# Kernel tuning notes

Measured on AMD Instinct MI355X. Metric: run time of the kernel, lower is better.

## Reference

```python
import jax, jax.numpy as jnp
import numpy as np

NUM_HEADS = 16


def setup_inputs() -> dict:
    key = jax.random.key(0)
    ks = jax.random.split(key, 5)
    S, B, N, C = 4, 2, 2048, 1024
    return {
        "x_all": jax.random.normal(ks[0], (S, B, N, C), dtype=jnp.float32),
        "w_qkv": jax.random.normal(ks[1], (C, 3 * C), dtype=jnp.float32) * (C ** -0.5),
        "b_qkv": jax.random.normal(ks[2], (3 * C,), dtype=jnp.float32) * 0.02,
        "w_proj": jax.random.normal(ks[3], (C, C), dtype=jnp.float32) * (C ** -0.5),
        "b_proj": jax.random.normal(ks[4], (C,), dtype=jnp.float32) * 0.02,
    }


def reference(x_all, w_qkv, b_qkv, w_proj, b_proj):
    # x_all: [S, B, N, C] -- S = cp_dim ring shards, each rank holds [B, N, C]
    S, B, N, C = x_all.shape
    H = NUM_HEADS
    D = C // H
    scale = 1.0 / np.sqrt(D).astype(np.float32)

    # same qkv projection on every rank
    qkv = (jnp.einsum("sbnc,ce->sbne", x_all, w_qkv) + b_qkv)
    qkv = qkv.reshape(S, B, N, 3, H, D)
    # rank 0's queries: [B, H, N, D]
    q = jnp.transpose(qkv[0, :, :, 0], (0, 2, 1, 3))
    # all shards' keys/values: [S, B, H, N, D]
    k = jnp.transpose(qkv[:, :, :, 1], (0, 1, 3, 2, 4))
    v = jnp.transpose(qkv[:, :, :, 2], (0, 1, 3, 2, 4))

    # ring loop: online softmax merge across KV shards (numerically stable
    # form of the source's exp(lse)-weighted average)
    attn_out, lse = None, None
    for s in range(S):
        scores = jnp.einsum("bhnd,bhmd->bhnm", q, k[s]) * scale  # [B,H,N,N]
        new_lse = jax.nn.logsumexp(scores, axis=-1)               # [B,H,N]
        probs = jnp.exp(scores - new_lse[..., None])
        new_out = jnp.einsum("bhnm,bhmd->bhnd", probs, v[s])      # [B,H,N,D]
        if attn_out is None:
            attn_out, lse = new_out, new_lse
        else:
            m = jnp.logaddexp(lse, new_lse)
            attn_out = (attn_out * jnp.exp(lse - m)[..., None]
                        + new_out * jnp.exp(new_lse - m)[..., None])
            lse = m

    # [B,H,N,D] -> [B,N,C]
    out = jnp.transpose(attn_out, (0, 2, 1, 3)).reshape(B, N, C)
    return out @ w_proj + b_proj
```

## Files before the change

### kernel.cpp

```cpp
#include <hip/hip_runtime.h>
#include <hip/hip_bf16.h>


typedef __bf16 bf16x8 __attribute__((ext_vector_type(8)));
typedef float v4f __attribute__((ext_vector_type(4)));

#if __has_builtin(__builtin_amdgcn_exp2f)
#define EXP2F(x) __builtin_amdgcn_exp2f(x)
#else
#define EXP2F(x) exp2f(x)
#endif

__device__ __forceinline__ float bf2f(unsigned short h) {
  union { unsigned int u; float f; } a; a.u = ((unsigned int)h) << 16; return a.f;
}
__device__ __forceinline__ unsigned short f2bf(float f) {
  union { float f; unsigned int u; } a; a.f = f;
  unsigned int u = a.u;
  unsigned int r = (u + 0x7fffu + ((u >> 16) & 1u)) >> 16;
  return (unsigned short)r;
}
__device__ __forceinline__ unsigned int pack2t(float a, float b) {
  union { float f; unsigned int u; } ua, ub; ua.f = a; ub.f = b;
  return (ua.u >> 16) | (ub.u & 0xffff0000u);
}
__device__ __forceinline__ bf16x8 ldfrag16(const unsigned short* p) {
  union { uint4 u; bf16x8 v; } x; x.u = *(const uint4*)p; return x.v;
}
__device__ __forceinline__ bf16x8 ones8() {
  union { unsigned short s[8]; bf16x8 v; } x;
#pragma unroll
  for (int i = 0; i < 8; i++) x.s[i] = 0x3F80;
  return x.v;
}
__device__ __forceinline__ void gld_lds16(const unsigned short* g, unsigned short* l) {
  __builtin_amdgcn_global_load_lds((__attribute__((address_space(1))) void*)g,
                                   (__attribute__((address_space(3))) void*)l, 16, 0, 0);
}

__global__ void detect_dtype(const unsigned short* __restrict__ x, int* flag) {
  __shared__ int cnt;
  if (threadIdx.x == 0) cnt = 0;
  __syncthreads();
  int sane = 0;
#pragma unroll
  for (int j = 0; j < 4; j++) {
    unsigned short v = x[2 * (threadIdx.x + 64 * j)];
    int e = (v >> 7) & 0xFF;
    if (e >= 90 && e <= 140) sane++;
  }
  atomicAdd(&cnt, sane);
  __syncthreads();
  if (threadIdx.x == 0) *flag = (cnt > 160) ? 0 : 1;
}

__global__ void conv_to_bf16(const void* __restrict__ in, unsigned short* __restrict__ out,
                             int n4, const int* __restrict__ flag) {
  int i = blockIdx.x * blockDim.x + threadIdx.x;
  if (i >= n4) return;
  if (*flag) {
    float4 v = ((const float4*)in)[i];
    ushort4 o;
    o.x = f2bf(v.x); o.y = f2bf(v.y); o.z = f2bf(v.z); o.w = f2bf(v.w);
    ((ushort4*)out)[i] = o;
  } else {
    ((ushort4*)out)[i] = ((const ushort4*)in)[i];
  }
}

__global__ void conv_bias(const void* __restrict__ bq_in, const void* __restrict__ bp_in,
                          unsigned short* __restrict__ bq, unsigned short* __restrict__ bp,
                          const int* __restrict__ flag) {
  int i = blockIdx.x * 256 + threadIdx.x;
  const void* in = (i < 768) ? bq_in : bp_in;
  unsigned short* out = (i < 768) ? bq : bp;
  int j = (i < 768) ? i : i - 768;
  if (*flag) {
    float4 v = ((const float4*)in)[j];
    ushort4 o;
    o.x = f2bf(v.x); o.y = f2bf(v.y); o.z = f2bf(v.z); o.w = f2bf(v.w);
    ((ushort4*)out)[j] = o;
  } else {
    ((ushort4*)out)[j] = ((const ushort4*)in)[j];
  }
}

__global__ void trans_both(const void* __restrict__ wqkv, const void* __restrict__ wproj,
                           unsigned short* __restrict__ wt1, unsigned short* __restrict__ wt2,
                           const int* __restrict__ flag) {
  __shared__ unsigned short t[32][33];
  int tx = threadIdx.x, ty = threadIdx.y;
  int bx = blockIdx.x;
  const void* in; unsigned short* out; int C, c0;
  if (bx < 96) { in = wqkv; out = wt1; C = 3072; c0 = bx * 32; }
  else         { in = wproj; out = wt2; C = 1024; c0 = (bx - 96) * 32; }
  const int R = 1024;
  int r0 = blockIdx.y * 32;
  int fp = *flag;
#pragma unroll
  for (int j = 0; j < 32; j += 8) {
    unsigned short v;
    if (fp) v = f2bf(((const float*)in)[(r0 + ty + j) * C + c0 + tx]);
    else    v = ((const unsigned short*)in)[(r0 + ty + j) * C + c0 + tx];
    t[ty + j][tx] = v;
  }
  __syncthreads();
#pragma unroll
  for (int j = 0; j < 32; j += 8) out[(c0 + ty + j) * R + r0 + tx] = t[tx][ty + j];
}

template <int MODE>
__launch_bounds__(256, 3)
__global__ void gemm_bt(const unsigned short* __restrict__ A,
                        const unsigned short* __restrict__ Bt,
                        const unsigned short* __restrict__ bias,
                        void* __restrict__ Cout,
                        int K, int ldc, const int* __restrict__ flag,
                        const unsigned short* Bt2, const unsigned short* bias2,
                        void* Cout2) {
  __shared__ unsigned short As[128 * 32];
  __shared__ unsigned short Bs[128 * 32];
  int tid = threadIdx.x;
  int w = tid >> 6, lane = tid & 63, col = lane & 15, quad = lane >> 4;
  int wm = w >> 1, wn = w & 1;
  int n0 = blockIdx.x * 128;
  int m0 = blockIdx.y * 128;
  const unsigned short* Bt_ = Bt;
  const unsigned short* bias_ = bias;
  void* Cout_ = Cout;
  bool isq = false;
  if constexpr (MODE == 3) {
    if (blockIdx.y >= 128) {
      m0 = (blockIdx.y - 128) * 128;
      Bt_ = Bt2; bias_ = bias2; Cout_ = Cout2;
      isq = true;
    }
  }
  int fp = 0;
  if constexpr (MODE == 2) fp = *flag;

  v4f acc[4][4];
#pragma unroll
  for (int i = 0; i < 4; i++)
#pragma unroll
    for (int j = 0; j < 4; j++) acc[i][j] = v4f{0.f, 0.f, 0.f, 0.f};

  int ra0 = tid >> 2, cc = tid & 3;
  const unsigned short* ga0 = &A[(m0 + ra0) * K + cc * 8];
  const unsigned short* ga1 = ga0 + 64 * K;
  const unsigned short* gb0 = &Bt_[(n0 + ra0) * K + cc * 8];
  const unsigned short* gb1 = gb0 + 64 * K;
  unsigned short* lA0 = &As[(w * 16) * 32];
  unsigned short* lA1 = &As[(64 + w * 16) * 32];
  unsigned short* lB0 = &Bs[(w * 16) * 32];
  unsigned short* lB1 = &Bs[(64 + w * 16) * 32];

  int niter = K >> 5;
  for (int it = 0; it < niter; it++) {
    __syncthreads();
    gld_lds16(ga0, lA0); gld_lds16(ga1, lA1);
    gld_lds16(gb0, lB0); gld_lds16(gb1, lB1);
    ga0 += 32; ga1 += 32; gb0 += 32; gb1 += 32;
    __syncthreads();
    bf16x8 af[4], bfr[4];
#pragma unroll
    for (int mi = 0; mi < 4; mi++) af[mi] = ldfrag16(&As[(wm * 64 + mi * 16 + col) * 32 + quad * 8]);
#pragma unroll
    for (int ni = 0; ni < 4; ni++) bfr[ni] = ldfrag16(&Bs[(wn * 64 + ni * 16 + col) * 32 + quad * 8]);
#pragma unroll
    for (int mi = 0; mi < 4; mi++)
#pragma unroll
      for (int ni = 0; ni < 4; ni++)
        acc[mi][ni] = __builtin_amdgcn_mfma_f32_16x16x32_bf16(af[mi], bfr[ni], acc[mi][ni], 0, 0, 0);
  }

  float bv[4];
#pragma unroll
  for (int ni = 0; ni < 4; ni++) bv[ni] = bf2f(bias_[n0 + wn * 64 + ni * 16 + col]);

  if constexpr (MODE == 1) {
    int rgb0 = m0 + wm * 64;
    int s = rgb0 >> 12, b = (rgb0 >> 11) & 1, n = rgb0 & 2047;
    int kvg0 = s * 2048 + n;
#pragma unroll
    for (int ni = 0; ni < 4; ni++) {
      int cg = n0 + wn * 64 + ni * 16 + col;
      int h = cg >> 6, d = cg & 63;
      unsigned short* rowp = &((unsigned short*)Cout_)[((b * 16 + h) * 64 + d) * 8192 + kvg0];
      float bvn = bv[ni];
#pragma unroll
      for (int r = 0; r < 4; r++) {
        ushort2 e, o2;
        e.x = f2bf(acc[0][ni][r] + bvn);
        e.y = f2bf(acc[2][ni][r] + bvn);
        o2.x = f2bf(acc[1][ni][r] + bvn);
        o2.y = f2bf(acc[3][ni][r] + bvn);
        *(ushort2*)&rowp[2 * (quad * 4 + r)] = e;
        *(ushort2*)&rowp[32 + 2 * (quad * 4 + r)] = o2;
      }
    }
  } else {
#pragma unroll
    for (int mi = 0; mi < 4; mi++)
#pragma unroll
      for (int ni = 0; ni < 4; ni++) {
        float vals[4];
#pragma unroll
        for (int r = 0; r < 4; r++) vals[r] = acc[mi][ni][r] + bv[ni];
        if constexpr (MODE == 3) {
          if (isq) {
#pragma unroll
            for (int r = 0; r < 4; r++) vals[r] *= 0.1803368801111601f;
          }
        }
        int rgb = m0 + wm * 64 + mi * 16 + quad * 4;
        int cg  = n0 + wn * 64 + ni * 16 + col;
        if constexpr (MODE == 0 || MODE == 3) {
          unsigned short* C = (unsigned short*)Cout_;
#pragma unroll
          for (int r = 0; r < 4; r++) C[(rgb + r) * ldc + cg] = f2bf(vals[r]);
        } else {
          if (fp) {
            float* C = (float*)Cout_;
#pragma unroll
            for (int r = 0; r < 4; r++) C[(rgb + r) * ldc + cg] = vals[r];
          } else {
            unsigned short* C = (unsigned short*)Cout_;
#pragma unroll
            for (int r = 0; r < 4; r++) C[(rgb + r) * ldc + cg] = f2bf(vals[r]);
          }
        }
      }
  }
}

__launch_bounds__(512, 4)
__global__ void attn_kernel(const unsigned short* __restrict__ qbuf,
                            const unsigned short* __restrict__ kbuf,
                            const unsigned short* __restrict__ vt,
                            float* __restrict__ po,
                            float* __restrict__ lbuf) {
  __shared__ unsigned short Ks[2][64 * 64];
  __shared__ unsigned short Vs[2][64 * 64];
  int tid = threadIdx.x;
  int w = tid >> 6, lane = tid & 63, col = lane & 15, quad = lane >> 4;
  int id = blockIdx.x;
  int xcd = id & 7, slot = id >> 3;
  int qt = slot & 7, gsub = slot >> 3;
  int g = gsub * 8 + xcd;
  int bh = g >> 1, half = g & 1;
  int b = bh >> 4, h = bh & 15;
  int q0 = qt * 256;

  bf16x8 aQ[2][2];
#pragma unroll
  for (int mj = 0; mj < 2; mj++)
#pragma unroll
    for (int kk = 0; kk < 2; kk++)
      aQ[mj][kk] = ldfrag16(&qbuf[(b * 2048 + q0 + w * 32 + mj * 16 + col) * 1024 +
                                  h * 64 + kk * 32 + quad * 8]);

  int r0 = tid >> 3, c0 = tid & 7;
  const unsigned short* kp = &kbuf[((half * 2) * 4096 + b * 2048 + r0) * 1024 + h * 64 + c0 * 8];
  const unsigned short* vp = &vt[(bh * 64 + r0) * 8192 + half * 4096 + c0 * 8];
  int sdst = r0 * 64 + 8 * (c0 ^ (r0 & 7));
  {
    uint4 k0 = *(const uint4*)kp, v0 = *(const uint4*)vp;
    *(uint4*)&Ks[0][sdst] = k0;
    *(uint4*)&Vs[0][sdst] = v0;
  }

  const bf16x8 vone = ones8();
  v4f o[2][4];
  v4f acc_l[2] = {v4f{0.f, 0.f, 0.f, 0.f}, v4f{0.f, 0.f, 0.f, 0.f}};
#pragma unroll
  for (int mj = 0; mj < 2; mj++)
#pragma unroll
    for (int di = 0; di < 4; di++) o[mj][di] = v4f{0.f, 0.f, 0.f, 0.f};

  __syncthreads();

  for (int kvt = 0; kvt < 64; kvt++) {
    int p = kvt & 1;
    uint4 pk, pv;
    if (kvt < 63) {
      int kstep = (((kvt + 1) & 31) == 0) ? (2048 + 64) * 1024 : 64 * 1024;
      kp += kstep; vp += 64;
      pk = *(const uint4*)kp; pv = *(const uint4*)vp;
    }

    v4f sc[4][2];
#pragma unroll
    for (int ni = 0; ni < 4; ni++)
#pragma unroll
      for (int mj = 0; mj < 2; mj++) sc[ni][mj] = v4f{0.f, 0.f, 0.f, 0.f};
#pragma unroll
    for (int kk = 0; kk < 2; kk++) {
      bf16x8 aK[4];
#pragma unroll
      for (int ni = 0; ni < 4; ni++) {
        int row = ni * 16 + col;
        aK[ni] = ldfrag16(&Ks[p][row * 64 + 8 * ((kk * 4 + quad) ^ (col & 7))]);
      }
#pragma unroll
      for (int ni = 0; ni < 4; ni++)
#pragma unroll
        for (int mj = 0; mj < 2; mj++)
          sc[ni][mj] = __builtin_amdgcn_mfma_f32_16x16x32_bf16(aK[ni], aQ[mj][kk], sc[ni][mj], 0, 0, 0);
    }

#pragma unroll
    for (int ni = 0; ni < 4; ni++)
#pragma unroll
      for (int mj = 0; mj < 2; mj++)
#pragma unroll
        for (int r = 0; r < 4; r++) sc[ni][mj][r] = EXP2F(sc[ni][mj][r]);

    bf16x8 aP[2][2];
#pragma unroll
    for (int mj = 0; mj < 2; mj++)
#pragma unroll
      for (int kk = 0; kk < 2; kk++) {
        union { unsigned int d[4]; bf16x8 v; } u;
#pragma unroll
        for (int t = 0; t < 4; t++)
          u.d[t] = pack2t(sc[kk][mj][t], sc[kk + 2][mj][t]);
        aP[mj][kk] = u.v;
      }

    if (kvt < 63) {
      *(uint4*)&Ks[p ^ 1][sdst] = pk;
      *(uint4*)&Vs[p ^ 1][sdst] = pv;
    }

#pragma unroll
    for (int kk = 0; kk < 2; kk++) {
#pragma unroll
      for (int mj = 0; mj < 2; mj++)
        acc_l[mj] = __builtin_amdgcn_mfma_f32_16x16x32_bf16(aP[mj][kk], vone, acc_l[mj], 0, 0, 0);
      bf16x8 bV[4];
#pragma unroll
      for (int di = 0; di < 4; di++) {
        int row = di * 16 + col;
        bV[di] = ldfrag16(&Vs[p][row * 64 + 8 * ((kk * 4 + quad) ^ (col & 7))]);
      }
#pragma unroll
      for (int mj = 0; mj < 2; mj++)
#pragma unroll
        for (int di = 0; di < 4; di++)
          o[mj][di] = __builtin_amdgcn_mfma_f32_16x16x32_bf16(aP[mj][kk], bV[di], o[mj][di], 0, 0, 0);
    }

    __syncthreads();
  }

  float* pb = po + half * 4194304;
#pragma unroll
  for (int mj = 0; mj < 2; mj++)
#pragma unroll
    for (int r = 0; r < 4; r++) {
      int n = q0 + w * 32 + mj * 16 + quad * 4 + r;
      if (col == 0) lbuf[half * 65536 + (b * 16 + h) * 2048 + n] = acc_l[mj][r];
#pragma unroll
      for (int di = 0; di < 4; di++) {
        int c = h * 64 + di * 16 + col;
        pb[(b * 2048 + n) * 1024 + c] = o[mj][di][r];
      }
    }
}

__global__ void merge_halves(const float* __restrict__ po, const float* __restrict__ lbuf,
                             unsigned short* __restrict__ attn) {
  int i = blockIdx.x * 256 + threadIdx.x;
  int r = i >> 8, c4 = i & 255;
  float l = lbuf[((r >> 11) * 16 + (c4 >> 4)) * 2048 + (r & 2047)] +
            lbuf[65536 + ((r >> 11) * 16 + (c4 >> 4)) * 2048 + (r & 2047)];
  float inv = 1.f / l;
  float4 a = ((const float4*)po)[i];
  float4 b = ((const float4*)po)[1048576 + i];
  ushort4 o;
  o.x = f2bf((a.x + b.x) * inv); o.y = f2bf((a.y + b.y) * inv);
  o.z = f2bf((a.z + b.z) * inv); o.w = f2bf((a.w + b.w) * inv);
  ((ushort4*)attn)[i] = o;
}

extern "C" void kernel_launch(void* const* d_in, const int* in_sizes, int n_in,
                              void* d_out, int out_size, void* d_ws, size_t ws_size,
                              hipStream_t stream) {
  const void* x      = d_in[0];
  const void* w_qkv  = d_in[1];
  const void* b_qkv  = d_in[2];
  const void* w_proj = d_in[3];
  const void* b_proj = d_in[4];

  char* ws = (char*)d_ws;
  unsigned short* xb   = (unsigned short*)(ws);
  unsigned short* kk   = (unsigned short*)(ws + 33554432);
  unsigned short* vt   = (unsigned short*)(ws + 67108864);
  unsigned short* q0b  = (unsigned short*)(ws + 100663296);
  unsigned short* attn = (unsigned short*)(ws + 109051904);
  unsigned short* wt1  = (unsigned short*)(ws + 117440512);
  unsigned short* wt2  = (unsigned short*)(ws + 123731968);
  unsigned short* bq   = (unsigned short*)(ws + 125829120);
  unsigned short* bp   = (unsigned short*)(ws + 125835264);
  int* flag            = (int*)(ws + 125837312);
  float* po   = (float*)xb;
  float* lbuf = (float*)wt1;

  detect_dtype<<<1, 64, 0, stream>>>((const unsigned short*)x, flag);

  conv_to_bf16<<<16384, 256, 0, stream>>>(x, xb, 4194304, flag);
  conv_bias<<<4, 256, 0, stream>>>(b_qkv, b_proj, bq, bp, flag);
  trans_both<<<dim3(128, 32), dim3(32, 8), 0, stream>>>(w_qkv, w_proj, wt1, wt2, flag);

  gemm_bt<3><<<dim3(8, 160), 256, 0, stream>>>(xb, wt1 + 1024 * 1024, bq + 1024, kk,
                                               1024, 1024, flag, wt1, bq, q0b);
  gemm_bt<1><<<dim3(8, 128), 256, 0, stream>>>(xb, wt1 + 2048 * 1024, bq + 2048, vt,
                                               1024, 0, flag, nullptr, nullptr, nullptr);

  attn_kernel<<<512, 512, 0, stream>>>(q0b, kk, vt, po, lbuf);
  merge_halves<<<4096, 256, 0, stream>>>(po, lbuf, attn);

  gemm_bt<2><<<dim3(8, 32), 256, 0, stream>>>(attn, wt2, bp, d_out,
                                              1024, 1024, flag, nullptr, nullptr, nullptr);
}
```

Baseline: 318.0 us.

## Software-pipeline attention loop: overlap QK^T of next tile with PV of previous

Restructures the attention KV loop so each iteration computes scores and exp for tile t while issuing the P·V MFMAs for tile t-1. V shared memory goes to a triple-buffer rotation so the previous tile's V stays resident while the next one loads. A prologue and epilogue handle the first and last tiles. The aim is to hide exp/pack latency behind MFMA work. It costs extra LDS and registers (aPn alongside aP), which may lower occupancy.

```diff
diff --git a/kernel.cpp b/kernel.cpp
--- a/kernel.cpp
+++ b/kernel.cpp
@@ -241,7 +241,7 @@
                             float* __restrict__ po,
                             float* __restrict__ lbuf) {
   __shared__ unsigned short Ks[2][64 * 64];
-  __shared__ unsigned short Vs[2][64 * 64];
+  __shared__ unsigned short Vs[3][64 * 64];
   int tid = threadIdx.x;
   int w = tid >> 6, lane = tid & 63, col = lane & 15, quad = lane >> 4;
   int id = blockIdx.x;
@@ -264,31 +264,26 @@
   const unsigned short* kp = &kbuf[((half * 2) * 4096 + b * 2048 + r0) * 1024 + h * 64 + c0 * 8];
   const unsigned short* vp = &vt[(bh * 64 + r0) * 8192 + half * 4096 + c0 * 8];
   int sdst = r0 * 64 + 8 * (c0 ^ (r0 & 7));
+
+  const bf16x8 vone = ones8();
+  v4f o[2][4];
+  v4f acc_l[2] = {v4f{0.f, 0.f, 0.f, 0.f}, v4f{0.f, 0.f, 0.f, 0.f}};
+#pragma unroll
+  for (int mj = 0; mj < 2; mj++)
+#pragma unroll
+    for (int di = 0; di < 4; di++) o[mj][di] = v4f{0.f, 0.f, 0.f, 0.f};
+
   {
     uint4 k0 = *(const uint4*)kp, v0 = *(const uint4*)vp;
     *(uint4*)&Ks[0][sdst] = k0;
     *(uint4*)&Vs[0][sdst] = v0;
   }
-
-  const bf16x8 vone = ones8();
-  v4f o[2][4];
-  v4f acc_l[2] = {v4f{0.f, 0.f, 0.f, 0.f}, v4f{0.f, 0.f, 0.f, 0.f}};
-#pragma unroll
-  for (int mj = 0; mj < 2; mj++)
-#pragma unroll
-    for (int di = 0; di < 4; di++) o[mj][di] = v4f{0.f, 0.f, 0.f, 0.f};
-
+  kp += 64 * 1024; vp += 64;
+  uint4 pk = *(const uint4*)kp, pv = *(const uint4*)vp;
   __syncthreads();
 
-  for (int kvt = 0; kvt < 64; kvt++) {
-    int p = kvt & 1;
-    uint4 pk, pv;
-    if (kvt < 63) {
-      int kstep = (((kvt + 1) & 31) == 0) ? (2048 + 64) * 1024 : 64 * 1024;
-      kp += kstep; vp += 64;
-      pk = *(const uint4*)kp; pv = *(const uint4*)vp;
-    }
-
+  bf16x8 aP[2][2];
+  {
     v4f sc[4][2];
 #pragma unroll
     for (int ni = 0; ni < 4; ni++)
@@ -300,7 +295,7 @@
 #pragma unroll
       for (int ni = 0; ni < 4; ni++) {
         int row = ni * 16 + col;
-        aK[ni] = ldfrag16(&Ks[p][row * 64 + 8 * ((kk * 4 + quad) ^ (col & 7))]);
+        aK[ni] = ldfrag16(&Ks[0][row * 64 + 8 * ((kk * 4 + quad) ^ (col & 7))]);
       }
 #pragma unroll
       for (int ni = 0; ni < 4; ni++)
@@ -308,15 +303,12 @@
         for (int mj = 0; mj < 2; mj++)
           sc[ni][mj] = __builtin_amdgcn_mfma_f32_16x16x32_bf16(aK[ni], aQ[mj][kk], sc[ni][mj], 0, 0, 0);
     }
-
 #pragma unroll
     for (int ni = 0; ni < 4; ni++)
 #pragma unroll
       for (int mj = 0; mj < 2; mj++)
 #pragma unroll
         for (int r = 0; r < 4; r++) sc[ni][mj][r] = EXP2F(sc[ni][mj][r]);
-
-    bf16x8 aP[2][2];
 #pragma unroll
     for (int mj = 0; mj < 2; mj++)
 #pragma unroll
@@ -327,10 +319,42 @@
           u.d[t] = pack2t(sc[kk][mj][t], sc[kk + 2][mj][t]);
         aP[mj][kk] = u.v;
       }
-
-    if (kvt < 63) {
-      *(uint4*)&Ks[p ^ 1][sdst] = pk;
-      *(uint4*)&Vs[p ^ 1][sdst] = pv;
+  }
+  *(uint4*)&Ks[1][sdst] = pk;
+  *(uint4*)&Vs[1][sdst] = pv;
+  __syncthreads();
+
+  const unsigned short* vprev = Vs[0];
+  const unsigned short* vcur  = Vs[1];
+  const unsigned short* vnext = Vs[2];
+
+  for (int t = 1; t < 64; t++) {
+    const unsigned short* kcur = Ks[t & 1];
+    unsigned short* knxt = (unsigned short*)Ks[(t + 1) & 1];
+    if (t < 63) {
+      int kstep = (((t + 1) & 31) == 0) ? (2048 + 64) * 1024 : 64 * 1024;
+      kp += kstep; vp += 64;
+      pk = *(const uint4*)kp; pv = *(const uint4*)vp;
+    }
+
+    v4f sc[4][2];
+#pragma unroll
+    for (int ni = 0; ni < 4; ni++)
+#pragma unroll
+      for (int mj = 0; mj < 2; mj++) sc[ni][mj] = v4f{0.f, 0.f, 0.f, 0.f};
+#pragma unroll
+    for (int kk = 0; kk < 2; kk++) {
+      bf16x8 aK[4];
+#pragma unroll
+      for (int ni = 0; ni < 4; ni++) {
+        int row = ni * 16 + col;
+        aK[ni] = ldfrag16(&kcur[row * 64 + 8 * ((kk * 4 + quad) ^ (col & 7))]);
+      }
+#pragma unroll
+      for (int ni = 0; ni < 4; ni++)
+#pragma unroll
+        for (int mj = 0; mj < 2; mj++)
+          sc[ni][mj] = __builtin_amdgcn_mfma_f32_16x16x32_bf16(aK[ni], aQ[mj][kk], sc[ni][mj], 0, 0, 0);
     }
 
 #pragma unroll
@@ -342,7 +366,7 @@
 #pragma unroll
       for (int di = 0; di < 4; di++) {
         int row = di * 16 + col;
-        bV[di] = ldfrag16(&Vs[p][row * 64 + 8 * ((kk * 4 + quad) ^ (col & 7))]);
+        bV[di] = ldfrag16(&vprev[row * 64 + 8 * ((kk * 4 + quad) ^ (col & 7))]);
       }
 #pragma unroll
       for (int mj = 0; mj < 2; mj++)
@@ -351,7 +375,55 @@
           o[mj][di] = __builtin_amdgcn_mfma_f32_16x16x32_bf16(aP[mj][kk], bV[di], o[mj][di], 0, 0, 0);
     }
 
+#pragma unroll
+    for (int ni = 0; ni < 4; ni++)
+#pragma unroll
+      for (int mj = 0; mj < 2; mj++)
+#pragma unroll
+        for (int r = 0; r < 4; r++) sc[ni][mj][r] = EXP2F(sc[ni][mj][r]);
+    bf16x8 aPn[2][2];
+#pragma unroll
+    for (int mj = 0; mj < 2; mj++)
+#pragma unroll
+      for (int kk = 0; kk < 2; kk++) {
+        union { unsigned int d[4]; bf16x8 v; } u;
+#pragma unroll
+        for (int tt = 0; tt < 4; tt++)
+          u.d[tt] = pack2t(sc[kk][mj][tt], sc[kk + 2][mj][tt]);
+        aPn[mj][kk] = u.v;
+      }
+
+    if (t < 63) {
+      *(uint4*)&knxt[sdst] = pk;
+      *(uint4*)&((unsigned short*)vnext)[sdst] = pv;
+    }
+
     __syncthreads();
+
+#pragma unroll
+    for (int mj = 0; mj < 2; mj++)
+#pragma unroll
+      for (int kk = 0; kk < 2; kk++) aP[mj][kk] = aPn[mj][kk];
+    const unsigned short* vt_ = vprev;
+    vprev = vcur; vcur = vnext; vnext = vt_;
+  }
+
+#pragma unroll
+  for (int kk = 0; kk < 2; kk++) {
+#pragma unroll
+    for (int mj = 0; mj < 2; mj++)
+      acc_l[mj] = __builtin_amdgcn_mfma_f32_16x16x32_bf16(aP[mj][kk], vone, acc_l[mj], 0, 0, 0);
+    bf16x8 bV[4];
+#pragma unroll
+    for (int di = 0; di < 4; di++) {
+      int row = di * 16 + col;
+      bV[di] = ldfrag16(&vprev[row * 64 + 8 * ((kk * 4 + quad) ^ (col & 7))]);
+    }
+#pragma unroll
+    for (int mj = 0; mj < 2; mj++)
+#pragma unroll
+      for (int di = 0; di < 4; di++)
+        o[mj][di] = __builtin_amdgcn_mfma_f32_16x16x32_bf16(aP[mj][kk], bV[di], o[mj][di], 0, 0, 0);
   }
 
   float* pb = po + half * 4194304;
```

Measured after the change: 314.2 us. No clear change (-1.2%).
